# Optimization experiments

Measured on AMD Instinct MI355X. Metric: run time of the kernel, lower is better.

## Reference

```python
import jax, jax.numpy as jnp
import numpy as np

N = 200000          # num_particles
E = 6400000         # num edges (avg degree 32)
ENV = 3             # env_dim
HIST = 15           # hist_v feature dim (5 steps * env_dim)
RADIUS = 0.05
VEL_MEAN = 0.0
VEL_STD = 1.0


def setup_inputs() -> dict:
    key = jax.random.key(0)
    k1, k2, k3, k4 = jax.random.split(key, 4)
    pos = jax.random.uniform(k1, (N, ENV), dtype=jnp.float32)
    hist_v = jax.random.normal(k2, (N, HIST), dtype=jnp.float32)
    src = jax.random.randint(k3, (E,), 0, N, dtype=jnp.int32)
    # offset in [1, N-1] guarantees no self-loops (rel_pos != 0)
    off = jax.random.randint(k4, (E,), 1, N, dtype=jnp.int32)
    dst = (src + off) % N
    boundary_info = jnp.array([0.0, 1.0, 0.0, 1.0, 0.0, 1.0], dtype=jnp.float32)
    return {"pos": pos, "hist_v": hist_v, "boundary_info": boundary_info,
            "src": src, "dst": dst}


def reference(pos, hist_v, boundary_info, src, dst):
    # node features
    current_v = hist_v[:, :ENV]                                  # [N, 3]
    normalized_v = (hist_v - VEL_MEAN) / VEL_STD                 # [N, 15]
    # pos repeat_interleave(2, dim=1): [x,x,y,y,z,z] minus per-dim lo/hi bounds
    pos2bound = jnp.repeat(pos, 2, axis=1) - boundary_info[None, :]  # [N, 6]
    normalized_pos2bound = jnp.clip(pos2bound / RADIUS, -1.0, 1.0)
    node_feature = jnp.concatenate([normalized_v, normalized_pos2bound], axis=1)  # [N, 21]

    # edge features: u_sub_v gather-subtract over edges
    rel_pos = (pos[src] - pos[dst]) / RADIUS                     # [E, 3]
    rel_dis = jnp.linalg.norm(rel_pos, axis=1, keepdims=True)    # [E, 1]
    edge_feature = jnp.concatenate([rel_pos, rel_dis], axis=1)   # [E, 4]

    return (node_feature.astype(jnp.float32),
            edge_feature.astype(jnp.float32),
            current_v.astype(jnp.float32))
```

## Files before the change

### kernel.cpp

```cpp
#include <hip/hip_runtime.h>
#include <math.h>


static constexpr float INV_R = 20.0f;

typedef float f32x4 __attribute__((ext_vector_type(4)));

__global__ void node_kernel(const float* __restrict__ pos,
                            const float* __restrict__ hist_v,
                            const float* __restrict__ bnd,
                            float* __restrict__ node_feat,
                            float* __restrict__ cur_v,
                            int n) {
    const int stride = gridDim.x * blockDim.x;
    const int tid = blockIdx.x * blockDim.x + threadIdx.x;

    const int total_nf = n * 21;
    for (int idx = tid; idx < total_nf; idx += stride) {
        const int node = idx / 21;
        const int c = idx - node * 21;
        float v;
        if (c < 15) {
            v = hist_v[node * 15 + c];
        } else {
            const int j = c - 15;
            const float p = pos[node * 3 + (j >> 1)];
            v = (p - bnd[j]) * INV_R;
            v = fminf(1.0f, fmaxf(-1.0f, v));
        }
        node_feat[idx] = v;
    }

    const int total_cv = n * 3;
    for (int idx = tid; idx < total_cv; idx += stride) {
        const int node = idx / 3;
        const int c = idx - node * 3;
        cur_v[idx] = hist_v[node * 15 + c];
    }
}

__global__ void edge_kernel(const float* __restrict__ pos,
                            const int* __restrict__ src,
                            const int* __restrict__ dst,
                            f32x4* __restrict__ edge_feat,
                            int e) {
    const int stride = gridDim.x * blockDim.x;
    for (int i = blockIdx.x * blockDim.x + threadIdx.x; i < e; i += stride) {
        const int s = src[i] * 3;
        const int d = dst[i] * 3;
        const float rx = (pos[s + 0] - pos[d + 0]) * INV_R;
        const float ry = (pos[s + 1] - pos[d + 1]) * INV_R;
        const float rz = (pos[s + 2] - pos[d + 2]) * INV_R;
        const float dis = sqrtf(rx * rx + ry * ry + rz * rz);
        f32x4 out = {rx, ry, rz, dis};
        __builtin_nontemporal_store(out, &edge_feat[i]);
    }
}

extern "C" void kernel_launch(void* const* d_in, const int* in_sizes, int n_in,
                              void* d_out, int out_size, void* d_ws, size_t ws_size,
                              hipStream_t stream) {
    const float* pos    = (const float*)d_in[0];
    const float* hist_v = (const float*)d_in[1];
    const float* bnd    = (const float*)d_in[2];
    const int*   src    = (const int*)d_in[3];
    const int*   dst    = (const int*)d_in[4];

    const int N = in_sizes[0] / 3;
    const int E = in_sizes[3];

    float* out       = (float*)d_out;
    float* node_feat = out;
    float* edge_feat = out + (size_t)N * 21;
    float* cur_v     = out + (size_t)N * 21 + (size_t)E * 4;

    const int block = 256;

    node_kernel<<<1024, block, 0, stream>>>(pos, hist_v, bnd, node_feat, cur_v, N);

    edge_kernel<<<2048, block, 0, stream>>>(pos, src, dst, (f32x4*)edge_feat, E);
}
```

Before: 258.3 us.

## Fuse node and edge kernels and process four edges per thread with vector loads

Merges the node and edge kernels into one launch, splitting work by block index so both run concurrently. Each edge thread now loads four src/dst indices as int4 vectors and gathers positions with a float2 plus scalar load, issuing more independent memory requests per thread. The grid-stride loop is replaced by a full grid sized to the edge count. It assumes the edge count is a multiple of four, with no tail handling.

```diff
diff --git a/kernel.cpp b/kernel.cpp
--- a/kernel.cpp
+++ b/kernel.cpp
@@ -5,55 +5,74 @@
 static constexpr float INV_R = 20.0f;
 
 typedef float f32x4 __attribute__((ext_vector_type(4)));
+typedef int   i32x4 __attribute__((ext_vector_type(4)));
+typedef float f32x2 __attribute__((ext_vector_type(2), aligned(4)));
 
-__global__ void node_kernel(const float* __restrict__ pos,
-                            const float* __restrict__ hist_v,
-                            const float* __restrict__ bnd,
-                            float* __restrict__ node_feat,
-                            float* __restrict__ cur_v,
-                            int n) {
-    const int stride = gridDim.x * blockDim.x;
-    const int tid = blockIdx.x * blockDim.x + threadIdx.x;
+__global__ __launch_bounds__(256) void fused_kernel(
+    const float* __restrict__ pos,
+    const float* __restrict__ hist_v,
+    const float* __restrict__ bnd,
+    const i32x4* __restrict__ src4,
+    const i32x4* __restrict__ dst4,
+    float* __restrict__ node_feat,
+    f32x4* __restrict__ edge_feat,
+    float* __restrict__ cur_v,
+    int n, int e4, int node_blocks)
+{
+    if ((int)blockIdx.x < node_blocks) {
+        const int stride = node_blocks * blockDim.x;
+        const int tid = blockIdx.x * blockDim.x + threadIdx.x;
 
-    const int total_nf = n * 21;
-    for (int idx = tid; idx < total_nf; idx += stride) {
-        const int node = idx / 21;
-        const int c = idx - node * 21;
-        float v;
-        if (c < 15) {
-            v = hist_v[node * 15 + c];
-        } else {
-            const int j = c - 15;
-            const float p = pos[node * 3 + (j >> 1)];
-            v = (p - bnd[j]) * INV_R;
-            v = fminf(1.0f, fmaxf(-1.0f, v));
+        const int total_nf = n * 21;
+        for (int idx = tid; idx < total_nf; idx += stride) {
+            const int node = idx / 21;
+            const int c = idx - node * 21;
+            float v;
+            if (c < 15) {
+                v = hist_v[node * 15 + c];
+            } else {
+                const int j = c - 15;
+                const float p = pos[node * 3 + (j >> 1)];
+                v = (p - bnd[j]) * INV_R;
+                v = fminf(1.0f, fmaxf(-1.0f, v));
+            }
+            node_feat[idx] = v;
         }
-        node_feat[idx] = v;
-    }
 
-    const int total_cv = n * 3;
-    for (int idx = tid; idx < total_cv; idx += stride) {
-        const int node = idx / 3;
-        const int c = idx - node * 3;
-        cur_v[idx] = hist_v[node * 15 + c];
-    }
-}
+        const int total_cv = n * 3;
+        for (int idx = tid; idx < total_cv; idx += stride) {
+            const int node = idx / 3;
+            const int c = idx - node * 3;
+            cur_v[idx] = hist_v[node * 15 + c];
+        }
+    } else {
+        const int t = (blockIdx.x - node_blocks) * blockDim.x + threadIdx.x;
+        if (t >= e4) return;
 
-__global__ void edge_kernel(const float* __restrict__ pos,
-                            const int* __restrict__ src,
-                            const int* __restrict__ dst,
-                            f32x4* __restrict__ edge_feat,
-                            int e) {
-    const int stride = gridDim.x * blockDim.x;
-    for (int i = blockIdx.x * blockDim.x + threadIdx.x; i < e; i += stride) {
-        const int s = src[i] * 3;
-        const int d = dst[i] * 3;
-        const float rx = (pos[s + 0] - pos[d + 0]) * INV_R;
-        const float ry = (pos[s + 1] - pos[d + 1]) * INV_R;
-        const float rz = (pos[s + 2] - pos[d + 2]) * INV_R;
-        const float dis = sqrtf(rx * rx + ry * ry + rz * rz);
-        f32x4 out = {rx, ry, rz, dis};
-        __builtin_nontemporal_store(out, &edge_feat[i]);
+        const i32x4 s4 = src4[t];
+        const i32x4 d4 = dst4[t];
+
+        float sx[4], sy[4], sz[4], dx[4], dy[4], dz[4];
+#pragma unroll
+        for (int k = 0; k < 4; ++k) {
+            const float* ps = pos + (size_t)s4[k] * 3;
+            const float* pd = pos + (size_t)d4[k] * 3;
+            const f32x2 sxy = *(const f32x2*)ps;
+            const float szv = ps[2];
+            const f32x2 dxy = *(const f32x2*)pd;
+            const float dzv = pd[2];
+            sx[k] = sxy.x; sy[k] = sxy.y; sz[k] = szv;
+            dx[k] = dxy.x; dy[k] = dxy.y; dz[k] = dzv;
+        }
+#pragma unroll
+        for (int k = 0; k < 4; ++k) {
+            const float rx = (sx[k] - dx[k]) * INV_R;
+            const float ry = (sy[k] - dy[k]) * INV_R;
+            const float rz = (sz[k] - dz[k]) * INV_R;
+            const float dis = sqrtf(rx * rx + ry * ry + rz * rz);
+            f32x4 o = {rx, ry, rz, dis};
+            __builtin_nontemporal_store(o, &edge_feat[4 * t + k]);
+        }
     }
 }
 
@@ -68,6 +87,7 @@
 
     const int N = in_sizes[0] / 3;
     const int E = in_sizes[3];
+    const int e4 = E / 4;
 
     float* out       = (float*)d_out;
     float* node_feat = out;
@@ -75,8 +95,10 @@
     float* cur_v     = out + (size_t)N * 21 + (size_t)E * 4;
 
     const int block = 256;
+    const int node_blocks = 1024;
+    const int edge_blocks = (e4 + block - 1) / block;
 
-    node_kernel<<<1024, block, 0, stream>>>(pos, hist_v, bnd, node_feat, cur_v, N);
-
-    edge_kernel<<<2048, block, 0, stream>>>(pos, src, dst, (f32x4*)edge_feat, E);
+    fused_kernel<<<node_blocks + edge_blocks, block, 0, stream>>>(
+        pos, hist_v, bnd, (const i32x4*)src, (const i32x4*)dst,
+        node_feat, (f32x4*)edge_feat, cur_v, N, e4, node_blocks);
 }
```

After: 243.9 us. 1.06x faster.
